# Optimization experiments

Hardware: AMD Instinct MI355X
Metric: run time of the kernel (lower is better)

## Reference

```python
import jax, jax.numpy as jnp
import numpy as np

B, S, DIM = 4, 2048, 2048
H, KVH, HD = 32, 8, 64
REPEATS = H // KVH
SCALE = HD ** -0.5


def _rope(x, cos, sin):
    # x: (B, S, Hn, HD); cos/sin: (S, HD//2)
    xr = x[..., 0::2]
    xi = x[..., 1::2]
    c = cos[:, None, :]  # (S, 1, HD//2) broadcasts over heads
    s = sin[:, None, :]
    out_r = xr * c - xi * s
    out_i = xr * s + xi * c
    return jnp.stack([out_r, out_i], axis=-1).reshape(x.shape)


def setup_inputs() -> dict:
    key = jax.random.key(0)
    ks = jax.random.split(key, 5)
    x = jax.random.normal(ks[0], (B, S, DIM), dtype=jnp.float32)
    wq = jax.random.normal(ks[1], (H * HD, DIM), dtype=jnp.float32) * 0.02
    wk = jax.random.normal(ks[2], (KVH * HD, DIM), dtype=jnp.float32) * 0.02
    wv = jax.random.normal(ks[3], (KVH * HD, DIM), dtype=jnp.float32) * 0.02
    wo = jax.random.normal(ks[4], (DIM, H * HD), dtype=jnp.float32) * 0.02
    # standard RoPE frequencies: freqs_cis = exp(i * t * theta)
    inv_freq = 1.0 / (10000.0 ** (jnp.arange(0, HD, 2, dtype=jnp.float32) / HD))
    angles = jnp.arange(S, dtype=jnp.float32)[:, None] * inv_freq[None, :]  # (S, HD//2)
    return {
        "x": x, "wq": wq, "wk": wk, "wv": wv, "wo": wo,
        "freqs_cos": jnp.cos(angles), "freqs_sin": jnp.sin(angles),
    }


def reference(x, wq, wk, wv, wo, freqs_cos, freqs_sin):
    b, s, _ = x.shape
    q = (x @ wq.T).reshape(b, s, H, HD)
    k = (x @ wk.T).reshape(b, s, KVH, HD)
    v = (x @ wv.T).reshape(b, s, KVH, HD)
    q = _rope(q, freqs_cos, freqs_sin)
    k = _rope(k, freqs_cos, freqs_sin)
    k_rep = jnp.repeat(k, REPEATS, axis=2)  # (B,S,H,HD)
    v_rep = jnp.repeat(v, REPEATS, axis=2)
    # NOTE: faithful to source - q is NOT transposed to (B,H,S,HD), so the
    # matmul contracts head_dim at each token, producing (B,S,H,H) scores
    # (mixing across heads per position), softmaxed over the last head axis.
    scores = jnp.einsum('bshd,bsed->bshe', q, k_rep) * SCALE  # (B,S,H,H)
    weights = jax.nn.softmax(scores, axis=-1)
    out = jnp.einsum('bshe,bsed->bshd', weights, v_rep)  # (B,S,H,HD)
    out = out.reshape(b, s, H * HD)
    return out @ wo.T
```

## Files before the change

kernel.cpp:

```cpp
#include <hip/hip_runtime.h>

typedef unsigned short u16;
typedef __bf16 bf16x8 __attribute__((ext_vector_type(8)));
typedef float f32x4 __attribute__((ext_vector_type(4)));

#define AS1 __attribute__((address_space(1)))
#define AS3 __attribute__((address_space(3)))

__device__ inline u16 f2bf(float f) {
    union { float f; unsigned u; } c; c.f = f;
    unsigned u = c.u;
    u += 0x7fffu + ((u >> 16) & 1u);
    return (u16)(u >> 16);
}
__device__ inline float bf2f(u16 b) {
    union { unsigned u; float f; } c; c.u = ((unsigned)b) << 16;
    return c.f;
}

__device__ inline void async_cp16(const void* g, void* l) {
    __builtin_amdgcn_global_load_lds((const AS1 void*)g, (AS3 void*)l, 16, 0, 0);
}

__global__ __launch_bounds__(256)
void conv_all(const float* __restrict__ x,
              const float* __restrict__ wq, const float* __restrict__ wk,
              const float* __restrict__ wv, const float* __restrict__ wo,
              u16* __restrict__ x_bf, u16* __restrict__ wqkv,
              u16* __restrict__ wo_bf) {
    int b = blockIdx.x;
    if (b < 8192) {
        int i = (b * 256 + threadIdx.x) * 8;
        float4 f0 = *(const float4*)(x + i);
        float4 f1 = *(const float4*)(x + i + 4);
        union { u16 h[8]; uint4 v; } o;
        o.h[0] = f2bf(f0.x); o.h[1] = f2bf(f0.y);
        o.h[2] = f2bf(f0.z); o.h[3] = f2bf(f0.w);
        o.h[4] = f2bf(f1.x); o.h[5] = f2bf(f1.y);
        o.h[6] = f2bf(f1.z); o.h[7] = f2bf(f1.w);
        *(uint4*)(x_bf + i) = o.v;
    } else {
        int i = ((b - 8192) * 256 + threadIdx.x) * 4;
        const float* src;
        u16* dst;
        if (i < 4194304)       { src = wq + i;           dst = wqkv + i; }
        else if (i < 5242880)  { src = wk + (i-4194304); dst = wqkv + i; }
        else if (i < 6291456)  { src = wv + (i-5242880); dst = wqkv + i; }
        else                   { src = wo + (i-6291456); dst = wo_bf + (i-6291456); }
        float4 f = *(const float4*)src;
        union { u16 h[4]; uint2 v; } o;
        o.h[0] = f2bf(f.x); o.h[1] = f2bf(f.y);
        o.h[2] = f2bf(f.z); o.h[3] = f2bf(f.w);
        *(uint2*)dst = o.v;
    }
}

template <int NI, bool BF16_OUT>
__global__ __launch_bounds__(512, 2)
void gemm_bt2(const u16* __restrict__ A, const u16* __restrict__ B,
              void* __restrict__ Cout, int N, int K) {
    constexpr int SZ = 32768 + NI * 8192;
    __shared__ __align__(16) char ldsc[2 * SZ];

    const int tid  = threadIdx.x;
    const int w    = tid >> 6;
    const int lane = tid & 63;
    const int row0 = blockIdx.x * 256;
    const int col0 = blockIdx.y * (NI * 64);
    const int wm = w >> 2, wn = w & 3;
    const int lm = lane & 15, quad = lane >> 4;

    const int NT  = K / 64;
    const int NIT = K / 128;
    const int K64 = K * 64;

    const int sr  = lane >> 3;
    const int stC = ((lane & 7) ^ sr) * 8;
    const u16* pA = A + (size_t)(row0 + w * 8 + sr) * K + stC;
    const u16* pB = B + (size_t)(col0 + w * 8 + sr) * K + stC;
    const int stagoff = w * 1024;

    const int cx0   = (quad ^ (lm & 7)) * 16;
    const int cx1   = cx0 ^ 64;
    const int aBase = (wm * 128 + lm) * 128;
    const int bBase = 32768 + (wn * (NI * 16) + lm) * 128;

    f32x4 acc[8][NI];
#pragma unroll
    for (int i = 0; i < 8; i++)
#pragma unroll
        for (int j = 0; j < NI; j++) acc[i][j] = (f32x4){0.f, 0.f, 0.f, 0.f};

    auto stage = [&](const u16* base, int v, int unit, int regionOff) {
        int kb = (v < NT ? v : NT - 1) * 64;
        async_cp16(base + (size_t)unit * K64 + kb,
                   ldsc + (v & 1) * SZ + regionOff + unit * 8192 + stagoff);
    };
#define ST_ALL(v)                                                             \
    {                                                                         \
        _Pragma("unroll")                                                     \
        for (int uu = 0; uu < 4; uu++) stage(pA, (v), uu, 0);                 \
        _Pragma("unroll")                                                     \
        for (int uu = 0; uu < NI; uu++) stage(pB, (v), uu, 32768);            \
    }

#define LDR(off) (*(const bf16x8*)(ldsc + (off)))
#define SB __builtin_amdgcn_sched_barrier(0)
#define BAR __builtin_amdgcn_s_barrier()
#define WLG0 asm volatile("s_waitcnt lgkmcnt(0)" ::: "memory")
#define WLG_S1INFLIGHT                                                        \
    do {                                                                      \
        if constexpr (NI == 3)                                                \
            asm volatile("s_waitcnt lgkmcnt(11)" ::: "memory");               \
        else                                                                  \
            asm volatile("s_waitcnt lgkmcnt(12)" ::: "memory");               \
    } while (0)
#define VMC                                                                   \
    do {                                                                      \
        if constexpr (NI == 3)                                                \
            asm volatile("s_waitcnt vmcnt(7)" ::: "memory");                  \
        else                                                                  \
            asm volatile("s_waitcnt vmcnt(8)" ::: "memory");                  \
    } while (0)

#define RD_HALF(S, BO, CXV)                                                   \
    {                                                                         \
        _Pragma("unroll")                                                     \
        for (int ni = 0; ni < NI; ni++)                                       \
            bgs[S][ni] = LDR((BO) + bBase + ni * 2048 + (CXV));               \
        _Pragma("unroll")                                                     \
        for (int mi = 0; mi < 8; mi++)                                        \
            af[S][mi] = LDR((BO) + aBase + mi * 2048 + (CXV));                \
    }
#define MFMA_TRAIN(S)                                                         \
    __builtin_amdgcn_s_setprio(1);                                            \
    _Pragma("unroll")                                                         \
    for (int mi = 0; mi < 8; mi++)                                            \
        _Pragma("unroll")                                                     \
        for (int ni = 0; ni < NI; ni++)                                       \
            acc[mi][ni] = __builtin_amdgcn_mfma_f32_16x16x32_bf16(            \
                af[S][mi], bgs[S][ni], acc[mi][ni], 0, 0, 0);                 \
    __builtin_amdgcn_s_setprio(0);

    bf16x8 bgs[2][NI], af[2][8];

    ST_ALL(0)
    ST_ALL(1)
    VMC;
    BAR;

#define TILE(u, BO)                                                           \
    {                                                                         \
        RD_HALF(0, BO, cx0)                                                   \
        SB;                                                                   \
        RD_HALF(1, BO, cx1)                                                   \
        SB;                                                                   \
        WLG_S1INFLIGHT;                                                       \
        SB;                                                                   \
        MFMA_TRAIN(0)                                                         \
        SB;                                                                   \
        WLG0;                                                                 \
        SB;                                                                   \
        BAR;                                                                  \
        ST_ALL((u) + 2)                                                       \
        SB;                                                                   \
        MFMA_TRAIN(1)                                                         \
        SB;                                                                   \
        VMC;                                                                  \
        BAR;                                                                  \
    }

    for (int it = 0; it < NIT; ++it) {
        const int t = 2 * it;
        TILE(t, 0)
        TILE(t + 1, SZ)
    }

#undef TILE
#undef MFMA_TRAIN
#undef RD_HALF
#undef VMC
#undef WLG_S1INFLIGHT
#undef WLG0
#undef BAR
#undef SB
#undef LDR
#undef ST_ALL

    const int rbase = row0 + wm * 128 + quad * 4;
    const int cbase = col0 + wn * (NI * 16) + lm;
    if (BF16_OUT) {
        u16* C = (u16*)Cout;
#pragma unroll
        for (int mi = 0; mi < 8; mi++)
#pragma unroll
            for (int r = 0; r < 4; r++) {
                size_t ro = (size_t)(rbase + mi * 16 + r) * N;
#pragma unroll
                for (int ni = 0; ni < NI; ni++)
                    C[ro + cbase + ni * 16] = f2bf(acc[mi][ni][r]);
            }
    } else {
        float* C = (float*)Cout;
#pragma unroll
        for (int mi = 0; mi < 8; mi++)
#pragma unroll
            for (int r = 0; r < 4; r++) {
                size_t ro = (size_t)(rbase + mi * 16 + r) * N;
#pragma unroll
                for (int ni = 0; ni < NI; ni++)
                    C[ro + cbase + ni * 16] = acc[mi][ni][r];
            }
    }
}

__global__ __launch_bounds__(256)
void attn_tok(const u16* __restrict__ qkv, u16* __restrict__ out) {
    __shared__ float kvf[1024];
    const int tok = blockIdx.x;
    const int t = threadIdx.x;
    const u16* qrow = qkv + (size_t)tok * 3072;

    {
        uint2 w = *(const uint2*)(qrow + 2048 + t * 4);
        kvf[t * 4 + 0] = bf2f((u16)(w.x & 0xffff));
        kvf[t * 4 + 1] = bf2f((u16)(w.x >> 16));
        kvf[t * 4 + 2] = bf2f((u16)(w.y & 0xffff));
        kvf[t * 4 + 3] = bf2f((u16)(w.y >> 16));
    }
    __syncthreads();

    const int h = t >> 3, j = t & 7;
    float qf[8];
    {
        uint4 w = *(const uint4*)(qrow + h * 64 + j * 8);
        unsigned ws4[4] = {w.x, w.y, w.z, w.w};
#pragma unroll
        for (int i = 0; i < 4; i++) {
            qf[2 * i]     = bf2f((u16)(ws4[i] & 0xffff));
            qf[2 * i + 1] = bf2f((u16)(ws4[i] >> 16));
        }
    }

    float s[8];
#pragma unroll
    for (int g = 0; g < 8; g++) {
        const float4* kk = (const float4*)(kvf + g * 64 + j * 8);
        float4 k0 = kk[0], k1 = kk[1];
        s[g] = qf[0] * k0.x + qf[1] * k0.y + qf[2] * k0.z + qf[3] * k0.w
             + qf[4] * k1.x + qf[5] * k1.y + qf[6] * k1.z + qf[7] * k1.w;
    }
#pragma unroll
    for (int g = 0; g < 8; g++) {
        s[g] += __shfl_xor(s[g], 1);
        s[g] += __shfl_xor(s[g], 2);
        s[g] += __shfl_xor(s[g], 4);
    }
    float m = -1e30f;
#pragma unroll
    for (int g = 0; g < 8; g++) { s[g] *= 0.125f; m = fmaxf(m, s[g]); }
    float p[8], l = 0.f;
#pragma unroll
    for (int g = 0; g < 8; g++) { p[g] = __expf(s[g] - m); l += p[g]; }
    float rl = 1.f / l;

    float o[8] = {0, 0, 0, 0, 0, 0, 0, 0};
#pragma unroll
    for (int g = 0; g < 8; g++) {
        float wgt = p[g] * rl;
        const float4* vv = (const float4*)(kvf + 512 + g * 64 + j * 8);
        float4 v0 = vv[0], v1 = vv[1];
        o[0] += wgt * v0.x; o[1] += wgt * v0.y;
        o[2] += wgt * v0.z; o[3] += wgt * v0.w;
        o[4] += wgt * v1.x; o[5] += wgt * v1.y;
        o[6] += wgt * v1.z; o[7] += wgt * v1.w;
    }

    unsigned po[4];
#pragma unroll
    for (int i = 0; i < 4; i++)
        po[i] = (unsigned)f2bf(o[2 * i]) | ((unsigned)f2bf(o[2 * i + 1]) << 16);
    uint4 wo_; wo_.x = po[0]; wo_.y = po[1]; wo_.z = po[2]; wo_.w = po[3];
    *(uint4*)(out + (size_t)tok * 2048 + h * 64 + j * 8) = wo_;
}

extern "C" void kernel_launch(void* const* d_in, const int* in_sizes, int n_in,
                              void* d_out, int out_size, void* d_ws, size_t ws_size,
                              hipStream_t stream) {
    const float* x  = (const float*)d_in[0];
    const float* wq = (const float*)d_in[1];
    const float* wk = (const float*)d_in[2];
    const float* wv = (const float*)d_in[3];
    const float* wo = (const float*)d_in[4];

    u16* x_bf  = (u16*)d_ws;
    u16* wqkv  = x_bf  + 16777216;
    u16* wo_bf = wqkv  + 6291456;
    u16* qkv   = wo_bf + 4194304;
    u16* attn  = x_bf;

    conv_all<<<18432, dim3(256), 0, stream>>>(x, wq, wk, wv, wo, x_bf, wqkv, wo_bf);

    gemm_bt2<3, true><<<dim3(32, 16), dim3(512), 0, stream>>>(x_bf, wqkv, qkv,
                                                              3072, 2048);

    attn_tok<<<8192, dim3(256), 0, stream>>>(qkv, attn);

    gemm_bt2<4, false><<<dim3(32, 8), dim3(512), 0, stream>>>(attn, wo_bf,
                                                              (float*)d_out,
                                                              2048, 2048);
}
```

Measured before the change: 323.2 us.

## Add dedicated QKV GEMM kernel with 256x384 tiles and 12 waves

Replaces the generic templated GEMM for the QKV projection with a specialized kernel. It uses 256x384 output tiles computed by 12 waves in a 2x6 layout, each wave owning a 128x64 sub-tile, with double-buffered async global-to-LDS staging done by 8 of the waves. The larger tile should raise data reuse per LDS load, cut redundant global reads, and make the grid exactly 256 blocks. In exchange it uses about 160KB of LDS per block, which limits each CU to one resident block and reduces latency hiding. Each thread also carries a large accumulator array.

```diff
diff --git a/kernel.cpp b/kernel.cpp
--- a/kernel.cpp
+++ b/kernel.cpp
@@ -55,6 +55,139 @@
     }
 }
 
+__global__ __launch_bounds__(768, 3)
+void gemm_qkv(const u16* __restrict__ A, const u16* __restrict__ B,
+              u16* __restrict__ Cout, int N, int K) {
+    constexpr int SZ = 81920;
+    __shared__ __align__(16) char ldsc[2 * SZ];
+
+    const int tid  = threadIdx.x;
+    const int w    = tid >> 6;
+    const int lane = tid & 63;
+    const int row0 = blockIdx.x * 256;
+    const int col0 = blockIdx.y * 384;
+    const int wm = w / 6, wn = w % 6;
+    const int lm = lane & 15, quad = lane >> 4;
+
+    const int NT  = K / 64;
+    const int NIT = K / 128;
+    const int K64 = K * 64;
+
+    const int sr  = lane >> 3;
+    const int stC = ((lane & 7) ^ sr) * 8;
+    const bool stager = (w < 8);
+    const u16* pA = A + (size_t)(row0 + (w & 7) * 8 + sr) * K + stC;
+    const u16* pB = B + (size_t)(col0 + (w & 7) * 8 + sr) * K + stC;
+    const int stagoff = (w & 7) * 1024;
+
+    const int cx0   = (quad ^ (lm & 7)) * 16;
+    const int cx1   = cx0 ^ 64;
+    const int aBase = (wm * 128 + lm) * 128;
+    const int bBase = 32768 + (wn * 64 + lm) * 128;
+
+    f32x4 acc[8][4];
+#pragma unroll
+    for (int i = 0; i < 8; i++)
+#pragma unroll
+        for (int j = 0; j < 4; j++) acc[i][j] = (f32x4){0.f, 0.f, 0.f, 0.f};
+
+    auto stage = [&](const u16* base, int v, int unit, int regionOff) {
+        int kb = (v < NT ? v : NT - 1) * 64;
+        async_cp16(base + (size_t)unit * K64 + kb,
+                   ldsc + (v & 1) * SZ + regionOff + unit * 8192 + stagoff);
+    };
+#define ST_ALL(v)                                                             \
+    if (stager) {                                                             \
+        _Pragma("unroll")                                                     \
+        for (int uu = 0; uu < 4; uu++) stage(pA, (v), uu, 0);                 \
+        _Pragma("unroll")                                                     \
+        for (int uu = 0; uu < 6; uu++) stage(pB, (v), uu, 32768);             \
+    }
+
+#define LDR(off) (*(const bf16x8*)(ldsc + (off)))
+#define SB __builtin_amdgcn_sched_barrier(0)
+#define BAR __builtin_amdgcn_s_barrier()
+#define WLG0 asm volatile("s_waitcnt lgkmcnt(0)" ::: "memory")
+#define WLG12 asm volatile("s_waitcnt lgkmcnt(12)" ::: "memory")
+#define VMC10 asm volatile("s_waitcnt vmcnt(10)" ::: "memory")
+
+#define RD_HALF(S, BO, CXV)                                                   \
+    {                                                                         \
+        _Pragma("unroll")                                                     \
+        for (int ni = 0; ni < 4; ni++)                                        \
+            bgs[S][ni] = LDR((BO) + bBase + ni * 2048 + (CXV));               \
+        _Pragma("unroll")                                                     \
+        for (int mi = 0; mi < 8; mi++)                                        \
+            af[S][mi] = LDR((BO) + aBase + mi * 2048 + (CXV));                \
+    }
+#define MFMA_TRAIN(S)                                                         \
+    __builtin_amdgcn_s_setprio(1);                                            \
+    _Pragma("unroll")                                                         \
+    for (int mi = 0; mi < 8; mi++)                                            \
+        _Pragma("unroll")                                                     \
+        for (int ni = 0; ni < 4; ni++)                                        \
+            acc[mi][ni] = __builtin_amdgcn_mfma_f32_16x16x32_bf16(            \
+                af[S][mi], bgs[S][ni], acc[mi][ni], 0, 0, 0);                 \
+    __builtin_amdgcn_s_setprio(0);
+
+    bf16x8 bgs[2][4], af[2][8];
+
+    ST_ALL(0)
+    ST_ALL(1)
+    VMC10;
+    BAR;
+
+#define TILE(u, BO)                                                           \
+    {                                                                         \
+        RD_HALF(0, BO, cx0)                                                   \
+        SB;                                                                   \
+        RD_HALF(1, BO, cx1)                                                   \
+        SB;                                                                   \
+        WLG12;                                                                \
+        SB;                                                                   \
+        MFMA_TRAIN(0)                                                         \
+        SB;                                                                   \
+        WLG0;                                                                 \
+        SB;                                                                   \
+        BAR;                                                                  \
+        ST_ALL((u) + 2)                                                       \
+        SB;                                                                   \
+        MFMA_TRAIN(1)                                                         \
+        SB;                                                                   \
+        VMC10;                                                                \
+        BAR;                                                                  \
+    }
+
+    for (int it = 0; it < NIT; ++it) {
+        const int t = 2 * it;
+        TILE(t, 0)
+        TILE(t + 1, SZ)
+    }
+
+#undef TILE
+#undef MFMA_TRAIN
+#undef RD_HALF
+#undef VMC10
+#undef WLG12
+#undef WLG0
+#undef BAR
+#undef SB
+#undef LDR
+#undef ST_ALL
+
+    const int rbase = row0 + wm * 128 + quad * 4;
+    const int cbase = col0 + wn * 64 + lm;
+#pragma unroll
+    for (int mi = 0; mi < 8; mi++)
+#pragma unroll
+        for (int r = 0; r < 4; r++) {
+            size_t ro = (size_t)(rbase + mi * 16 + r) * N;
+#pragma unroll
+            for (int ni = 0; ni < 4; ni++)
+                Cout[ro + cbase + ni * 16] = f2bf(acc[mi][ni][r]);
+        }
+}
+
 template <int NI, bool BF16_OUT>
 __global__ __launch_bounds__(512, 2)
 void gemm_bt2(const u16* __restrict__ A, const u16* __restrict__ B,
@@ -301,8 +434,7 @@
 
     conv_all<<<18432, dim3(256), 0, stream>>>(x, wq, wk, wv, wo, x_bf, wqkv, wo_bf);
 
-    gemm_bt2<3, true><<<dim3(32, 16), dim3(512), 0, stream>>>(x_bf, wqkv, qkv,
-                                                              3072, 2048);
+    gemm_qkv<<<dim3(32, 8), dim3(768), 0, stream>>>(x_bf, wqkv, qkv, 3072, 2048);
 
     attn_tok<<<8192, dim3(256), 0, stream>>>(qkv, attn);
 
```

Result: slower. 1.188 ms (+267.7%).
